# Kernel optimization log

Hardware: AMD Instinct MI355X
Metric: run time of the kernel (lower is better)

Reference implementation:

```python
import jax, jax.numpy as jnp
import numpy as np

B, SQ, SE, SI, SEI = 16, 512, 512, 256, 768
D, H = 1024, 16
DK = D // H
L1, L2 = 0.5, 0.5
NEG = -1e30  # stand-in for -inf masked_fill


def setup_inputs() -> dict:
    key = jax.random.key(0)
    ks = jax.random.split(key, 32)
    f = lambda i, shp: jax.random.normal(ks[i], shp, dtype=jnp.float32)
    w = lambda i: f(i, (D, D)) * (1.0 / np.sqrt(D))
    b = lambda i: jnp.zeros((D,), jnp.float32)
    inp = {
        'q': f(0, (B, SQ, D)),
        'k_e': f(1, (B, SE, D)), 'v_e': f(2, (B, SE, D)),
        'k_i': f(3, (B, SI, D)), 'v_i': f(4, (B, SI, D)),
        'k_ei': f(5, (B, SEI, D)), 'v_ei': f(6, (B, SEI, D)),
        'mask_e': jax.random.randint(ks[7], (B, SQ, SE), 0, 2) == 1,
        'mask_ei': jax.random.randint(ks[8], (B, SQ, SEI), 0, 2) == 1,
        'e_padding_mask': jax.random.randint(ks[9], (B, SE), 0, 2) == 1,
        'ei_padding_mask': jax.random.randint(ks[10], (B, SEI), 0, 2) == 1,
        'Wq': w(11), 'bq': b(11),
        'Wke': w(12), 'bke': b(12), 'Wve': w(13), 'bve': b(13),
        'Wki': w(14), 'bki': b(14), 'Wvi': w(15), 'bvi': b(15),
        'Wkei': w(16), 'bkei': b(16), 'Wvei': w(17), 'bvei': b(17),
        'Wout': w(18), 'bout': b(18),
    }
    return inp


def _proj(x, W, b):
    # (B, S, D) -> (B, H, S, DK)
    B_, S_, _ = x.shape
    return (x @ W + b).reshape(B_, S_, H, DK).transpose(0, 2, 1, 3)


def _attn(qh, kh, vh, mask, pad_mask):
    # qh: (B,H,Sq,DK), kh/vh: (B,H,Sk,DK)
    s = jnp.einsum('bhqd,bhkd->bhqk', qh, kh) / np.sqrt(DK)
    if mask is not None:
        s = jnp.where(mask[:, None, :, :], NEG, s)
    if pad_mask is not None:
        s = jnp.where(pad_mask[:, None, None, :], NEG, s)
    w = jax.nn.softmax(s, axis=-1)
    # dropout in original is applied to a discarded temp (eval / no-op)
    return jnp.einsum('bhqk,bhkd->bhqd', w, vh), w


def reference(q, k_e, k_i, k_ei, v_e, v_i, v_ei,
              mask_e, mask_ei, e_padding_mask, ei_padding_mask,
              Wq, bq, Wke, bke, Wve, bve, Wki, bki, Wvi, bvi,
              Wkei, bkei, Wvei, bvei, Wout, bout):
    qh = _proj(q, Wq, bq)
    o_e, aw_e = _attn(qh, _proj(k_e, Wke, bke), _proj(v_e, Wve, bve), mask_e, e_padding_mask)
    o_i, aw_i = _attn(qh, _proj(k_i, Wki, bki), _proj(v_i, Wvi, bvi), None, None)
    o_ei, _ = _attn(qh, _proj(k_ei, Wkei, bkei), _proj(v_ei, Wvei, bvei), mask_ei, ei_padding_mask)
    scores = o_e + L1 * o_i + L2 * o_ei  # (B,H,Sq,DK)
    concat = scores.transpose(0, 2, 1, 3).reshape(B, SQ, D)
    output = concat @ Wout + bout
    return output, aw_e, aw_i
```

## Files before the change

### kernel.cpp

```cpp
#include <hip/hip_runtime.h>
#include <stdint.h>

typedef __attribute__((ext_vector_type(8))) short bf16x8;
typedef __attribute__((ext_vector_type(4))) short s16x4;
typedef __attribute__((ext_vector_type(4))) float f32x4;

__device__ __forceinline__ short f2bf(float f){
  unsigned x = __float_as_uint(f);
  unsigned r = (x + 0x7fffu + ((x >> 16) & 1u)) >> 16;
  return (short)r;
}

__device__ __forceinline__ void g2l16(const void* g, void* l){
  __builtin_amdgcn_global_load_lds(
      (const __attribute__((address_space(1))) unsigned int*)(unsigned long long)(uintptr_t)g,
      (__attribute__((address_space(3))) unsigned int*)(unsigned int)(uintptr_t)l,
      16, 0, 0);
}

struct C4 { const float* in[4]; short* out[4]; int n8[4]; };
__global__ __launch_bounds__(256) void cvt4(C4 c){
  const int z = blockIdx.z;
  const int i = blockIdx.x * 256 + threadIdx.x;
  if (i >= c.n8[z]) return;
  const float4* p = (const float4*)c.in[z] + (size_t)i * 2;
  const float4 a = p[0], b = p[1];
  bf16x8 v;
  v[0] = f2bf(a.x); v[1] = f2bf(a.y); v[2] = f2bf(a.z); v[3] = f2bf(a.w);
  v[4] = f2bf(b.x); v[5] = f2bf(b.y); v[6] = f2bf(b.z); v[7] = f2bf(b.w);
  *(bf16x8*)(c.out[z] + (size_t)i * 8) = v;
}

__global__ __launch_bounds__(256)
void make_bits(const int* __restrict__ mask, const int* __restrict__ pad,
               unsigned* __restrict__ bits, int SK){
  const int s = blockIdx.x * 256 + threadIdx.x;
  const size_t row = blockIdx.y;
  const int b = (int)(row >> 9);
  const bool v = (mask[row * SK + s] != 0) || (pad[(size_t)b * SK + s] != 0);
  unsigned long long bal = __ballot(v);
  const int lane = threadIdx.x & 63;
  if ((lane & 31) == 0)
    bits[(row * SK + s) >> 5] = (unsigned)(bal >> (lane & 32));
}

struct W8 { const float* w[8]; };
__global__ __launch_bounds__(256) void pack_w8(W8 ws8, short* __restrict__ out){
  const int m = blockIdx.y;
  const float* __restrict__ W = ws8.w[m];
  short* o = out + (size_t)m * 1048576 + (size_t)blockIdx.x * 4096;
  const int kt = blockIdx.x & 31, nt = blockIdx.x >> 5;
  const int t = threadIdx.x;
  #pragma unroll
  for (int i = 0; i < 16; ++i){
    int flat = i * 256 + t;
    int kl = flat >> 7;
    int nl = flat & 127;
    o[nl * 32 + kl] = f2bf(W[(size_t)(kt * 32 + kl) * 1024 + nt * 128 + nl]);
  }
}

struct GSeg { const short* A; const short* Wp; const float* bias; void* C; int om; int S; int mt; };
struct G4 { GSeg s[4]; };
__global__ __launch_bounds__(256)
void gemm128b(G4 g){
  const GSeg sg = g.s[blockIdx.z];
  if (blockIdx.x >= sg.mt) return;
  __shared__ short sA[2][4096];
  __shared__ short sB[2][4096];
  const int t = threadIdx.x;
  const int m0 = blockIdx.x * 128;
  const int nt = blockIdx.y;
  const int n0 = nt * 128;
  const int w = t >> 6, lane = t & 63, lr = lane & 15, lg = lane >> 4;
  const int wm = (w >> 1) * 64, wn = (w & 1) * 64;

  const int arow  = t >> 2;
  const int acol8 = (t & 3) * 8;
  const short* Ag = sg.A + (size_t)(m0 + arow) * 1024 + acol8;
  const short* Bg = sg.Wp + (size_t)nt * 32 * 4096 + t * 8;

  f32x4 acc[4][4] = {};

  {
    g2l16(Ag, sA[0] + t * 8);
    g2l16(Ag + 64 * 1024, sA[0] + 2048 + t * 8);
    g2l16(Bg, sB[0] + t * 8);
    g2l16(Bg + 2048, sB[0] + 2048 + t * 8);
  }

  int cur = 0;
  for (int kt = 0; kt < 32; ++kt){
    __syncthreads();
    if (kt < 31){
      const int kn = kt + 1;
      g2l16(Ag + kn * 32, sA[cur ^ 1] + t * 8);
      g2l16(Ag + 64 * 1024 + kn * 32, sA[cur ^ 1] + 2048 + t * 8);
      const short* bt = Bg + (size_t)kn * 4096;
      g2l16(bt, sB[cur ^ 1] + t * 8);
      g2l16(bt + 2048, sB[cur ^ 1] + 2048 + t * 8);
    }

    bf16x8 af[4], bfr[4];
    #pragma unroll
    for (int mi = 0; mi < 4; ++mi)
      af[mi] = *(const bf16x8*)&sA[cur][(wm + mi * 16 + lr) * 32 + lg * 8];
    #pragma unroll
    for (int ni = 0; ni < 4; ++ni)
      bfr[ni] = *(const bf16x8*)&sB[cur][(wn + ni * 16 + lr) * 32 + lg * 8];
    #pragma unroll
    for (int mi = 0; mi < 4; ++mi)
      #pragma unroll
      for (int ni = 0; ni < 4; ++ni)
        acc[mi][ni] = __builtin_amdgcn_mfma_f32_16x16x32_bf16(
            af[mi], bfr[ni], acc[mi][ni], 0, 0, 0);
    cur ^= 1;
  }

  #pragma unroll
  for (int ni = 0; ni < 4; ++ni){
    const int n = n0 + wn + ni * 16 + lr;
    const float bv = sg.bias[n];
    #pragma unroll
    for (int mi = 0; mi < 4; ++mi){
      const int mb = m0 + wm + mi * 16 + lg * 4;
      if (sg.om == 0){
        short* C = (short*)sg.C;
        #pragma unroll
        for (int j = 0; j < 4; ++j)
          C[(size_t)(mb + j) * 1024 + n] = f2bf(acc[mi][ni][j] + bv);
      } else if (sg.om == 1){
        short* C = (short*)sg.C;
        const int bb = mb / sg.S, sb = mb % sg.S;
        const int hh = n >> 6, dk = n & 63;
        s16x4 pk;
        #pragma unroll
        for (int j = 0; j < 4; ++j) pk[j] = f2bf(acc[mi][ni][j] + bv);
        *(s16x4*)&C[(((size_t)bb * 16 + hh) * 64 + dk) * sg.S + sb] = pk;
      } else {
        float* C = (float*)sg.C;
        #pragma unroll
        for (int j = 0; j < 4; ++j)
          C[(size_t)(mb + j) * 1024 + n] = acc[mi][ni][j] + bv;
      }
    }
  }
}

template<int SK, bool HAS_BIAS, bool SINGLE>
__device__ __forceinline__ void attn_mod(
    const short* __restrict__ Kp, const short* __restrict__ Vt,
    const unsigned* __restrict__ bits, float* __restrict__ aw,
    const bf16x8 (&qf)[2], f32x4 (&tot)[4], float wgt,
    short* sK, short* sV, short* sPw,
    int b, int h, int qw, int w, int lane, int lr, int lg){
  constexpr int NT  = SK / 128;
  constexpr int SKW = SK / 32;

  const int kchunk = (lane & 7) ^ ((lane >> 3) & 7);
  const short* Ksrc = Kp + ((size_t)b * SK + w * 16 + (lane >> 3)) * 1024 + h * 64 + kchunk * 8;
  short* sKd = sK + w * 1024 + lane * 8;
  short* sVd = sV + w * 1024 + lane * 8;
  const short* Vsrc = Vt + ((size_t)(b * 16 + h)) * 64 * SK;

  const unsigned* bitrow[4];
  if (HAS_BIAS){
    #pragma unroll
    for (int j = 0; j < 4; ++j)
      bitrow[j] = bits + ((size_t)(b * 512 + qw + lg * 4 + j)) * SKW;
  }

  float lrow[4];
  #pragma unroll
  for (int j = 0; j < 4; ++j) lrow[j] = 0.f;
  f32x4 acco[4] = {};

  if (!SINGLE){
    for (int tt = 0; tt < NT; ++tt){
      const int s0 = tt * 128;
      __syncthreads();
      g2l16(Ksrc + (size_t)s0 * 1024, sKd);
      g2l16(Ksrc + (size_t)(s0 + 8) * 1024, sKd + 512);
      __syncthreads();

      f32x4 accs[8];
      #pragma unroll
      for (int si = 0; si < 8; ++si){
        f32x4 a = {};
        #pragma unroll
        for (int dt = 0; dt < 2; ++dt){
          bf16x8 kf = *(const bf16x8*)&sK[(si * 16 + lr) * 64 + ((dt * 4 + lg) ^ (lr & 7)) * 8];
          a = __builtin_amdgcn_mfma_f32_16x16x32_bf16(qf[dt], kf, a, 0, 0, 0);
        }
        accs[si] = a;
      }

      #pragma unroll
      for (int j = 0; j < 4; ++j){
        unsigned wb[4];
        if (HAS_BIAS){
          #pragma unroll
          for (int sp = 0; sp < 4; ++sp) wb[sp] = bitrow[j][(s0 >> 5) + sp];
        }
        float ssum = 0.f;
        #pragma unroll
        for (int si = 0; si < 8; ++si){
          float v = accs[si][j] * 0.125f;
          if (HAS_BIAS && ((wb[si >> 1] >> ((si & 1) * 16 + lr)) & 1u)) v = -1e30f;
          ssum += __expf(v);
        }
        lrow[j] += ssum;
      }
    }

    #pragma unroll
    for (int j = 0; j < 4; ++j){
      #pragma unroll
      for (int d = 1; d < 16; d <<= 1) lrow[j] += __shfl_xor(lrow[j], d);
    }
    float rinv[4];
    #pragma unroll
    for (int j = 0; j < 4; ++j) rinv[j] = lrow[j] > 0.f ? 1.0f / lrow[j] : 0.f;

    for (int tt = 0; tt < NT; ++tt){
      const int s0 = tt * 128;
      __syncthreads();
      g2l16(Ksrc + (size_t)s0 * 1024, sKd);
      g2l16(Ksrc + (size_t)(s0 + 8) * 1024, sKd + 512);
      #pragma unroll
      for (int i = 0; i < 2; ++i){
        const int dd = w * 8 + i * 4 + (lane >> 4);
        const int cg = (lane & 15) ^ (dd & 15);
        g2l16(Vsrc + (size_t)dd * SK + s0 + cg * 8, sVd + i * 512);
      }
      __syncthreads();

      f32x4 accs[8];
      #pragma unroll
      for (int si = 0; si < 8; ++si){
        f32x4 a = {};
        #pragma unroll
        for (int dt = 0; dt < 2; ++dt){
          bf16x8 kf = *(const bf16x8*)&sK[(si * 16 + lr) * 64 + ((dt * 4 + lg) ^ (lr & 7)) * 8];
          a = __builtin_amdgcn_mfma_f32_16x16x32_bf16(qf[dt], kf, a, 0, 0, 0);
        }
        accs[si] = a;
      }

      #pragma unroll
      for (int half = 0; half < 2; ++half){
        #pragma unroll
        for (int j = 0; j < 4; ++j){
          unsigned wb[2];
          if (HAS_BIAS){
            #pragma unroll
            for (int sp = 0; sp < 2; ++sp) wb[sp] = bitrow[j][(s0 >> 5) + half * 2 + sp];
          }
          const int qq = lg * 4 + j;
          float* awrow = aw + (((size_t)(b * 16 + h)) * 512 + qw + qq) * SK + s0 + half * 64 + lr;
          #pragma unroll
          for (int si2 = 0; si2 < 4; ++si2){
            const int si = half * 4 + si2;
            float v = accs[si][j] * 0.125f;
            if (HAS_BIAS && ((wb[si2 >> 1] >> ((si2 & 1) * 16 + lr)) & 1u)) v = -1e30f;
            const float p = __expf(v) * rinv[j];
            __builtin_nontemporal_store(p, &awrow[si2 * 16]);
            sPw[qq * 64 + (((si2 * 2 + (lr >> 3)) ^ (qq & 7)) * 8) + (lr & 7)] = f2bf(p);
          }
        }
        #pragma unroll
        for (int kt2 = 0; kt2 < 2; ++kt2){
          const int kt = half * 2 + kt2;
          bf16x8 pa = *(const bf16x8*)&sPw[lr * 64 + (((kt2 * 4 + lg) ^ (lr & 7)) * 8)];
          #pragma unroll
          for (int ni = 0; ni < 4; ++ni){
            bf16x8 vf = *(const bf16x8*)&sV[(ni * 16 + lr) * 128 + ((kt * 4 + lg) ^ lr) * 8];
            acco[ni] = __builtin_amdgcn_mfma_f32_16x16x32_bf16(pa, vf, acco[ni], 0, 0, 0);
          }
        }
      }
    }

    #pragma unroll
    for (int ni = 0; ni < 4; ++ni)
      #pragma unroll
      for (int j = 0; j < 4; ++j)
        tot[ni][j] += wgt * acco[ni][j];
  } else {
    for (int tt = 0; tt < NT; ++tt){
      const int s0 = tt * 128;
      __syncthreads();
      g2l16(Ksrc + (size_t)s0 * 1024, sKd);
      g2l16(Ksrc + (size_t)(s0 + 8) * 1024, sKd + 512);
      #pragma unroll
      for (int i = 0; i < 2; ++i){
        const int dd = w * 8 + i * 4 + (lane >> 4);
        const int cg = (lane & 15) ^ (dd & 15);
        g2l16(Vsrc + (size_t)dd * SK + s0 + cg * 8, sVd + i * 512);
      }
      __syncthreads();

      f32x4 accs[8];
      #pragma unroll
      for (int si = 0; si < 8; ++si){
        f32x4 a = {};
        #pragma unroll
        for (int dt = 0; dt < 2; ++dt){
          bf16x8 kf = *(const bf16x8*)&sK[(si * 16 + lr) * 64 + ((dt * 4 + lg) ^ (lr & 7)) * 8];
          a = __builtin_amdgcn_mfma_f32_16x16x32_bf16(qf[dt], kf, a, 0, 0, 0);
        }
        accs[si] = a;
      }

      #pragma unroll
      for (int half = 0; half < 2; ++half){
        #pragma unroll
        for (int j = 0; j < 4; ++j){
          unsigned wb[2];
          if (HAS_BIAS){
            #pragma unroll
            for (int sp = 0; sp < 2; ++sp) wb[sp] = bitrow[j][(s0 >> 5) + half * 2 + sp];
          }
          const int qq = lg * 4 + j;
          float ls = 0.f;
          #pragma unroll
          for (int si2 = 0; si2 < 4; ++si2){
            const int si = half * 4 + si2;
            float v = accs[si][j] * 0.125f;
            if (HAS_BIAS && ((wb[si2 >> 1] >> ((si2 & 1) * 16 + lr)) & 1u)) v = -1e30f;
            const float p = __expf(v);
            ls += p;
            sPw[qq * 64 + (((si2 * 2 + (lr >> 3)) ^ (qq & 7)) * 8) + (lr & 7)] = f2bf(p);
          }
          lrow[j] += ls;
        }
        #pragma unroll
        for (int kt2 = 0; kt2 < 2; ++kt2){
          const int kt = half * 2 + kt2;
          bf16x8 pa = *(const bf16x8*)&sPw[lr * 64 + (((kt2 * 4 + lg) ^ (lr & 7)) * 8)];
          #pragma unroll
          for (int ni = 0; ni < 4; ++ni){
            bf16x8 vf = *(const bf16x8*)&sV[(ni * 16 + lr) * 128 + ((kt * 4 + lg) ^ lr) * 8];
            acco[ni] = __builtin_amdgcn_mfma_f32_16x16x32_bf16(pa, vf, acco[ni], 0, 0, 0);
          }
        }
      }
    }

    #pragma unroll
    for (int j = 0; j < 4; ++j){
      #pragma unroll
      for (int d = 1; d < 16; d <<= 1) lrow[j] += __shfl_xor(lrow[j], d);
      const float r = lrow[j] > 0.f ? wgt / lrow[j] : 0.f;
      #pragma unroll
      for (int ni = 0; ni < 4; ++ni) tot[ni][j] += r * acco[ni][j];
    }
  }
}

__global__ __launch_bounds__(512)
void attn_fused(const short* __restrict__ Qp,
                const short* __restrict__ Kep, const short* __restrict__ Vte,
                const unsigned* __restrict__ bits_e, float* __restrict__ aw_e,
                const short* __restrict__ Kip, const short* __restrict__ Vti,
                float* __restrict__ aw_i,
                const short* __restrict__ Keip, const short* __restrict__ Vtei,
                const unsigned* __restrict__ bits_ei,
                short* __restrict__ concat){
  __shared__ short sK[8192];
  __shared__ short sV[8192];
  __shared__ short sP[8192];

  const int bid = blockIdx.x;
  const int qt = bid >> 8;
  const int g  = bid & 255;
  const int h = g & 15, b = g >> 4;
  const int q0 = qt * 128;
  const int t = threadIdx.x, w = t >> 6, lane = t & 63;
  const int lr = lane & 15, lg = lane >> 4;
  const int qw = q0 + w * 16;
  short* sPw = sP + w * 1024;

  const short* Qb = Qp + ((size_t)(b * 512 + qw + lr)) * 1024 + h * 64;
  bf16x8 qf[2];
  qf[0] = *(const bf16x8*)&Qb[lg * 8];
  qf[1] = *(const bf16x8*)&Qb[32 + lg * 8];

  f32x4 tot[4] = {};

  attn_mod<512, true , false>(Kep,  Vte,  bits_e,  aw_e, qf, tot, 1.0f,
                              sK, sV, sPw, b, h, qw, w, lane, lr, lg);
  attn_mod<256, false, false>(Kip,  Vti,  nullptr, aw_i, qf, tot, 0.5f,
                              sK, sV, sPw, b, h, qw, w, lane, lr, lg);
  attn_mod<768, true , true >(Keip, Vtei, bits_ei, nullptr, qf, tot, 0.5f,
                              sK, sV, sPw, b, h, qw, w, lane, lr, lg);

  #pragma unroll
  for (int ni = 0; ni < 4; ++ni)
    #pragma unroll
    for (int j = 0; j < 4; ++j){
      const size_t addr = ((size_t)(b * 512 + qw + lg * 4 + j)) * 1024 + h * 64 + ni * 16 + lr;
      concat[addr] = f2bf(tot[ni][j]);
    }
}

extern "C" void kernel_launch(void* const* d_in, const int* in_sizes, int n_in,
                              void* d_out, int out_size, void* d_ws, size_t ws_size,
                              hipStream_t stream){
  const float* q    = (const float*)d_in[0];
  const float* k_e  = (const float*)d_in[1];
  const float* v_e  = (const float*)d_in[2];
  const float* k_i  = (const float*)d_in[3];
  const float* v_i  = (const float*)d_in[4];
  const float* k_ei = (const float*)d_in[5];
  const float* v_ei = (const float*)d_in[6];
  const int* mask_e  = (const int*)d_in[7];
  const int* mask_ei = (const int*)d_in[8];
  const int* pad_e   = (const int*)d_in[9];
  const int* pad_ei  = (const int*)d_in[10];
  const float* Wq   = (const float*)d_in[11]; const float* bq   = (const float*)d_in[12];
  const float* Wke  = (const float*)d_in[13]; const float* bke  = (const float*)d_in[14];
  const float* Wve  = (const float*)d_in[15]; const float* bve  = (const float*)d_in[16];
  const float* Wki  = (const float*)d_in[17]; const float* bki  = (const float*)d_in[18];
  const float* Wvi  = (const float*)d_in[19]; const float* bvi  = (const float*)d_in[20];
  const float* Wkei = (const float*)d_in[21]; const float* bkei = (const float*)d_in[22];
  const float* Wvei = (const float*)d_in[23]; const float* bvei = (const float*)d_in[24];
  const float* Wout = (const float*)d_in[25]; const float* bout = (const float*)d_in[26];

  char* ws = (char*)d_ws;
  const size_t MB = 1048576;
  short* PW     = (short*)(ws);
  short* StA0   = (short*)(ws + 16 * MB);
  short* StA1   = (short*)(ws + 32 * MB);
  short* StA2   = (short*)(ws + 48 * MB);
  short* StB0   = (short*)(ws + 16 * MB);
  short* StB1   = (short*)(ws + 24 * MB);
  short* StC0   = (short*)(ws + 32 * MB);
  short* StC1   = (short*)(ws + 56 * MB);
  unsigned* bits_e  = (unsigned*)(ws + 80 * MB);
  unsigned* bits_ei = (unsigned*)(ws + 82 * MB);
  short* Qp     = (short*)(ws + 85 * MB);
  short* Kep    = (short*)(ws + 101 * MB);
  short* Kip    = (short*)(ws + 117 * MB);
  short* Keip   = (short*)(ws + 125 * MB);
  short* Vte    = (short*)(ws + 149 * MB);
  short* Vti    = (short*)(ws + 165 * MB);
  short* Vtei   = (short*)(ws + 173 * MB);
  short* concat = (short*)(ws + 16 * MB);

  float* out0 = (float*)d_out;
  float* aw_e = out0 + 8388608;
  float* aw_i = out0 + 75497472;

  W8 w8;
  w8.w[0] = Wq;  w8.w[1] = Wke;  w8.w[2] = Wve;  w8.w[3] = Wki;
  w8.w[4] = Wvi; w8.w[5] = Wkei; w8.w[6] = Wvei; w8.w[7] = Wout;
  pack_w8<<<dim3(256, 8), 256, 0, stream>>>(w8, PW);

  {
    C4 c;
    c.in[0] = q;   c.out[0] = StA0; c.n8[0] = 1048576;
    c.in[1] = k_e; c.out[1] = StA1; c.n8[1] = 1048576;
    c.in[2] = v_e; c.out[2] = StA2; c.n8[2] = 1048576;
    c.in[3] = q;   c.out[3] = StA0; c.n8[3] = 0;
    cvt4<<<dim3(4096, 1, 3), 256, 0, stream>>>(c);
    G4 gg;
    gg.s[0] = {StA0, PW + 0 * 1048576, bq,  Qp,  0, 512, 64};
    gg.s[1] = {StA1, PW + 1 * 1048576, bke, Kep, 0, 512, 64};
    gg.s[2] = {StA2, PW + 2 * 1048576, bve, Vte, 1, 512, 64};
    gg.s[3] = gg.s[0];
    gemm128b<<<dim3(64, 8, 3), 256, 0, stream>>>(gg);
  }
  {
    C4 c;
    c.in[0] = k_i;  c.out[0] = StB0; c.n8[0] = 524288;
    c.in[1] = v_i;  c.out[1] = StB1; c.n8[1] = 524288;
    c.in[2] = k_ei; c.out[2] = StC0; c.n8[2] = 1572864;
    c.in[3] = v_ei; c.out[3] = StC1; c.n8[3] = 1572864;
    cvt4<<<dim3(6144, 1, 4), 256, 0, stream>>>(c);
    G4 gg;
    gg.s[0] = {StB0, PW + 3 * 1048576, bki,  Kip,  0, 256, 32};
    gg.s[1] = {StB1, PW + 4 * 1048576, bvi,  Vti,  1, 256, 32};
    gg.s[2] = {StC0, PW + 5 * 1048576, bkei, Keip, 0, 768, 96};
    gg.s[3] = {StC1, PW + 6 * 1048576, bvei, Vtei, 1, 768, 96};
    gemm128b<<<dim3(96, 8, 4), 256, 0, stream>>>(gg);
  }

  make_bits<<<dim3(2, 8192), 256, 0, stream>>>(mask_e,  pad_e,  bits_e,  512);
  make_bits<<<dim3(3, 8192), 256, 0, stream>>>(mask_ei, pad_ei, bits_ei, 768);

  attn_fused<<<1024, 512, 0, stream>>>(Qp, Kep, Vte, bits_e, aw_e,
                                       Kip, Vti, aw_i, Keip, Vtei, bits_ei, concat);

  {
    G4 gg;
    gg.s[0] = {concat, PW + 7 * 1048576, bout, out0, 2, 512, 64};
    gg.s[1] = gg.s[0]; gg.s[2] = gg.s[0]; gg.s[3] = gg.s[0];
    gemm128b<<<dim3(64, 8, 1), 256, 0, stream>>>(gg);
  }
}
```

Baseline: 542.0 us.

## Double-buffer K/V tiles in LDS to overlap loads with attention compute

The shared K and V tiles are doubled so the next 128-key tile is prefetched with async global-to-LDS loads while the current tile is processed. This removes one of the two block barriers per iteration in all three attention loops. The parity of NT is relied on so that the first tile of the second pass can go into buffer 0 without an extra barrier. LDS use per block grows from 48KB to 80KB, which may reduce how many blocks fit on a CU.

```diff
diff --git a/kernel.cpp b/kernel.cpp
--- a/kernel.cpp
+++ b/kernel.cpp
@@ -156,12 +156,12 @@
     int b, int h, int qw, int w, int lane, int lr, int lg){
   constexpr int NT  = SK / 128;
   constexpr int SKW = SK / 32;
+  static_assert((NT & 1) == 0, "buffer-parity argument needs even NT");
 
   const int kchunk = (lane & 7) ^ ((lane >> 3) & 7);
   const short* Ksrc = Kp + ((size_t)b * SK + w * 16 + (lane >> 3)) * 1024 + h * 64 + kchunk * 8;
-  short* sKd = sK + w * 1024 + lane * 8;
-  short* sVd = sV + w * 1024 + lane * 8;
   const short* Vsrc = Vt + ((size_t)(b * 16 + h)) * 64 * SK;
+  const int ldoff = w * 1024 + lane * 8;
 
   const unsigned* bitrow[4];
   if (HAS_BIAS){
@@ -175,13 +175,26 @@
   for (int j = 0; j < 4; ++j) lrow[j] = 0.f;
   f32x4 acco[4] = {};
 
+#define SKB(c) (sK + (c) * 8192)
+#define SVB(c) (sV + (c) * 8192)
+#define STAGE_K(c, s0) do{ \
+    g2l16(Ksrc + (size_t)(s0) * 1024, SKB(c) + ldoff); \
+    g2l16(Ksrc + (size_t)((s0) + 8) * 1024, SKB(c) + ldoff + 512); }while(0)
+#define STAGE_V(c, s0) do{ \
+    const int dd0 = w * 8 + (lane >> 4); \
+    const int cg0 = (lane & 15) ^ (dd0 & 15); \
+    g2l16(Vsrc + (size_t)dd0 * SK + (s0) + cg0 * 8, SVB(c) + ldoff); \
+    const int dd1 = dd0 + 4; \
+    const int cg1 = (lane & 15) ^ (dd1 & 15); \
+    g2l16(Vsrc + (size_t)dd1 * SK + (s0) + cg1 * 8, SVB(c) + ldoff + 512); }while(0)
+
   if (!SINGLE){
+    STAGE_K(0, 0);
+    int cur = 0;
     for (int tt = 0; tt < NT; ++tt){
-      const int s0 = tt * 128;
       __syncthreads();
-      g2l16(Ksrc + (size_t)s0 * 1024, sKd);
-      g2l16(Ksrc + (size_t)(s0 + 8) * 1024, sKd + 512);
-      __syncthreads();
+      if (tt + 1 < NT) STAGE_K(cur ^ 1, (tt + 1) * 128);
+      const short* kb = SKB(cur);
 
       f32x4 accs[8];
       #pragma unroll
@@ -189,7 +202,7 @@
         f32x4 a = {};
         #pragma unroll
         for (int dt = 0; dt < 2; ++dt){
-          bf16x8 kf = *(const bf16x8*)&sK[(si * 16 + lr) * 64 + ((dt * 4 + lg) ^ (lr & 7)) * 8];
+          bf16x8 kf = *(const bf16x8*)&kb[(si * 16 + lr) * 64 + ((dt * 4 + lg) ^ (lr & 7)) * 8];
           a = __builtin_amdgcn_mfma_f32_16x16x32_bf16(qf[dt], kf, a, 0, 0, 0);
         }
         accs[si] = a;
@@ -200,7 +213,7 @@
         unsigned wb[4];
         if (HAS_BIAS){
           #pragma unroll
-          for (int sp = 0; sp < 4; ++sp) wb[sp] = bitrow[j][(s0 >> 5) + sp];
+          for (int sp = 0; sp < 4; ++sp) wb[sp] = bitrow[j][tt * 4 + sp];
         }
         float ssum = 0.f;
         #pragma unroll
@@ -211,6 +224,7 @@
         }
         lrow[j] += ssum;
       }
+      cur ^= 1;
     }
 
     #pragma unroll
@@ -222,18 +236,15 @@
     #pragma unroll
     for (int j = 0; j < 4; ++j) rinv[j] = lrow[j] > 0.f ? 1.0f / lrow[j] : 0.f;
 
+    STAGE_K(0, 0);
+    STAGE_V(0, 0);
+    cur = 0;
     for (int tt = 0; tt < NT; ++tt){
       const int s0 = tt * 128;
       __syncthreads();
-      g2l16(Ksrc + (size_t)s0 * 1024, sKd);
-      g2l16(Ksrc + (size_t)(s0 + 8) * 1024, sKd + 512);
-      #pragma unroll
-      for (int i = 0; i < 2; ++i){
-        const int dd = w * 8 + i * 4 + (lane >> 4);
-        const int cg = (lane & 15) ^ (dd & 15);
-        g2l16(Vsrc + (size_t)dd * SK + s0 + cg * 8, sVd + i * 512);
-      }
-      __syncthreads();
+      if (tt + 1 < NT){ STAGE_K(cur ^ 1, s0 + 128); STAGE_V(cur ^ 1, s0 + 128); }
+      const short* kb = SKB(cur);
+      const short* vb = SVB(cur);
 
       f32x4 accs[8];
       #pragma unroll
@@ -241,7 +252,7 @@
         f32x4 a = {};
         #pragma unroll
         for (int dt = 0; dt < 2; ++dt){
-          bf16x8 kf = *(const bf16x8*)&sK[(si * 16 + lr) * 64 + ((dt * 4 + lg) ^ (lr & 7)) * 8];
+          bf16x8 kf = *(const bf16x8*)&kb[(si * 16 + lr) * 64 + ((dt * 4 + lg) ^ (lr & 7)) * 8];
           a = __builtin_amdgcn_mfma_f32_16x16x32_bf16(qf[dt], kf, a, 0, 0, 0);
         }
         accs[si] = a;
@@ -254,7 +265,7 @@
           unsigned wb[2];
           if (HAS_BIAS){
             #pragma unroll
-            for (int sp = 0; sp < 2; ++sp) wb[sp] = bitrow[j][(s0 >> 5) + half * 2 + sp];
+            for (int sp = 0; sp < 2; ++sp) wb[sp] = bitrow[j][tt * 4 + half * 2 + sp];
           }
           const int qq = lg * 4 + j;
           float* awrow = aw + (((size_t)(b * 16 + h)) * 512 + qw + qq) * SK + s0 + half * 64 + lr;
@@ -274,11 +285,12 @@
           bf16x8 pa = *(const bf16x8*)&sPw[lr * 64 + (((kt2 * 4 + lg) ^ (lr & 7)) * 8)];
           #pragma unroll
           for (int ni = 0; ni < 4; ++ni){
-            bf16x8 vf = *(const bf16x8*)&sV[(ni * 16 + lr) * 128 + ((kt * 4 + lg) ^ lr) * 8];
+            bf16x8 vf = *(const bf16x8*)&vb[(ni * 16 + lr) * 128 + ((kt * 4 + lg) ^ lr) * 8];
             acco[ni] = __builtin_amdgcn_mfma_f32_16x16x32_bf16(pa, vf, acco[ni], 0, 0, 0);
           }
         }
       }
+      cur ^= 1;
     }
 
     #pragma unroll
@@ -287,18 +299,15 @@
       for (int j = 0; j < 4; ++j)
         tot[ni][j] += wgt * acco[ni][j];
   } else {
+    STAGE_K(0, 0);
+    STAGE_V(0, 0);
+    int cur = 0;
     for (int tt = 0; tt < NT; ++tt){
       const int s0 = tt * 128;
       __syncthreads();
-      g2l16(Ksrc + (size_t)s0 * 1024, sKd);
-      g2l16(Ksrc + (size_t)(s0 + 8) * 1024, sKd + 512);
-      #pragma unroll
-      for (int i = 0; i < 2; ++i){
-        const int dd = w * 8 + i * 4 + (lane >> 4);
-        const int cg = (lane & 15) ^ (dd & 15);
-        g2l16(Vsrc + (size_t)dd * SK + s0 + cg * 8, sVd + i * 512);
-      }
-      __syncthreads();
+      if (tt + 1 < NT){ STAGE_K(cur ^ 1, s0 + 128); STAGE_V(cur ^ 1, s0 + 128); }
+      const short* kb = SKB(cur);
+      const short* vb = SVB(cur);
 
       f32x4 accs[8];
       #pragma unroll
@@ -306,7 +315,7 @@
         f32x4 a = {};
         #pragma unroll
         for (int dt = 0; dt < 2; ++dt){
-          bf16x8 kf = *(const bf16x8*)&sK[(si * 16 + lr) * 64 + ((dt * 4 + lg) ^ (lr & 7)) * 8];
+          bf16x8 kf = *(const bf16x8*)&kb[(si * 16 + lr) * 64 + ((dt * 4 + lg) ^ (lr & 7)) * 8];
           a = __builtin_amdgcn_mfma_f32_16x16x32_bf16(qf[dt], kf, a, 0, 0, 0);
         }
         accs[si] = a;
@@ -319,7 +328,7 @@
           unsigned wb[2];
           if (HAS_BIAS){
             #pragma unroll
-            for (int sp = 0; sp < 2; ++sp) wb[sp] = bitrow[j][(s0 >> 5) + half * 2 + sp];
+            for (int sp = 0; sp < 2; ++sp) wb[sp] = bitrow[j][tt * 4 + half * 2 + sp];
           }
           const int qq = lg * 4 + j;
           float ls = 0.f;
@@ -340,11 +349,12 @@
           bf16x8 pa = *(const bf16x8*)&sPw[lr * 64 + (((kt2 * 4 + lg) ^ (lr & 7)) * 8)];
           #pragma unroll
           for (int ni = 0; ni < 4; ++ni){
-            bf16x8 vf = *(const bf16x8*)&sV[(ni * 16 + lr) * 128 + ((kt * 4 + lg) ^ lr) * 8];
+            bf16x8 vf = *(const bf16x8*)&vb[(ni * 16 + lr) * 128 + ((kt * 4 + lg) ^ lr) * 8];
             acco[ni] = __builtin_amdgcn_mfma_f32_16x16x32_bf16(pa, vf, acco[ni], 0, 0, 0);
           }
         }
       }
+      cur ^= 1;
     }
 
     #pragma unroll
@@ -356,6 +366,10 @@
       for (int ni = 0; ni < 4; ++ni) tot[ni][j] += r * acco[ni][j];
     }
   }
+#undef SKB
+#undef SVB
+#undef STAGE_K
+#undef STAGE_V
 }
 
 __global__ __launch_bounds__(512)
@@ -367,8 +381,8 @@
                 const short* __restrict__ Keip, const short* __restrict__ Vtei,
                 const unsigned* __restrict__ bits_ei,
                 short* __restrict__ concat){
-  __shared__ short sK[8192];
-  __shared__ short sV[8192];
+  __shared__ short sK[2 * 8192];
+  __shared__ short sV[2 * 8192];
   __shared__ short sP[8192];
 
   const int bid = blockIdx.x;
```

Measured after the change: 524.1 us. -3.3%, faster.
